# Kernel tuning notes

Measured on AMD Instinct MI355X. Metric: run time of the kernel, lower is better.

Reference implementation:

```python
import jax, jax.numpy as jnp
import numpy as np

N = 50000      # nodes
E = 800000     # edges (avg degree 16)
F_IN = 64      # node_feature_space
H = 64         # hidden_dim
G = 16         # graphs in batch
BN_EPS = 1e-5


def setup_inputs() -> dict:
    key = jax.random.key(0)
    ks = jax.random.split(key, 8)
    x = jax.random.normal(ks[0], (N, F_IN), jnp.float32)
    edge_index = jax.random.randint(ks[1], (2, E), 0, N, dtype=jnp.int64)
    batch = jnp.sort(jax.random.randint(ks[2], (N,), 0, G, dtype=jnp.int64))
    init = lambda k, shp, fan: jax.random.normal(k, shp, jnp.float32) / np.float32(np.sqrt(fan))
    params = dict(
        W1_0=init(ks[3], (F_IN, H), F_IN), b1_0=jnp.zeros((H,), jnp.float32),
        W2_0=init(ks[4], (H, H), H),       b2_0=jnp.zeros((H,), jnp.float32),
        g_0=jnp.ones((H,), jnp.float32),   be_0=jnp.zeros((H,), jnp.float32),
        W1_1=init(ks[5], (H, H), H),       b1_1=jnp.zeros((H,), jnp.float32),
        W2_1=init(ks[6], (H, H), H),       b2_1=jnp.zeros((H,), jnp.float32),
        g_1=jnp.ones((H,), jnp.float32),   be_1=jnp.zeros((H,), jnp.float32),
    )
    return dict(x=x, edge_index=edge_index, batch=batch, **params)


def _gin_layer(x, src, dst, W1, b1, W2, b2, g, be):
    # GINConv (eps=0): h_i = MLP(x_i + sum_{j->i} x_j)
    agg = jax.ops.segment_sum(x[src], dst, num_segments=N)   # [N, d]
    h = x + agg
    h = jnp.maximum(h @ W1 + b1, 0.0) @ W2 + b2              # Linear-ReLU-Linear
    # BatchNorm1d (training-mode batch stats, biased variance as in torch)
    mu = h.mean(axis=0)
    var = h.var(axis=0)
    h = (h - mu) * jax.lax.rsqrt(var + BN_EPS) * g + be
    return jnp.maximum(h, 0.0)                               # ReLU


def reference(x, edge_index, batch,
              W1_0, b1_0, W2_0, b2_0, g_0, be_0,
              W1_1, b1_1, W2_1, b2_1, g_1, be_1):
    src, dst = edge_index[0], edge_index[1]
    x = _gin_layer(x, src, dst, W1_0, b1_0, W2_0, b2_0, g_0, be_0)
    x = _gin_layer(x, src, dst, W1_1, b1_1, W2_1, b2_1, g_1, be_1)
    # global_mean_pool over graph ids
    cnt = jax.ops.segment_sum(jnp.ones((N,), x.dtype), batch, num_segments=G)
    sums = jax.ops.segment_sum(x, batch, num_segments=G)
    h_graph = sums / jnp.maximum(cnt, 1.0)[:, None]
    return (x, h_graph)
```

## Files before the change

kernel.cpp:

```cpp
#include <hip/hip_runtime.h>
#include <hip/hip_bf16.h>


constexpr int NN = 50000;
constexpr int NE = 800000;
constexpr int HD = 64;
constexpr int NG = 16;
constexpr float BN_EPS = 1e-5f;
constexpr int SCAN_BLOCKS = (NN + 255) / 256;
constexpr int NBUCK = (NN + 1023) / 1024;
constexpr int BIN1_BLOCKS = (NE + 4095) / 4096;

__global__ __launch_bounds__(256)
void count_kernel(const int* __restrict__ ei, int* __restrict__ cnt) {
    int e = blockIdx.x * 256 + threadIdx.x;
    if (e >= NE) return;
    atomicAdd(&cnt[ei[NE + e]], 1);
}

__global__ __launch_bounds__(256)
void scan1_kernel(const int* __restrict__ cnt, int* __restrict__ row_ptr,
                  int* __restrict__ partials) {
    int i = blockIdx.x * 256 + threadIdx.x;
    int v = (i < NN) ? cnt[i] : 0;
    __shared__ int s[256];
    s[threadIdx.x] = v;
    __syncthreads();
#pragma unroll
    for (int off = 1; off < 256; off <<= 1) {
        int add = (threadIdx.x >= off) ? s[threadIdx.x - off] : 0;
        __syncthreads();
        s[threadIdx.x] += add;
        __syncthreads();
    }
    if (i < NN) row_ptr[i] = s[threadIdx.x] - v;
    if (threadIdx.x == 255) partials[blockIdx.x] = s[255];
}

__global__ __launch_bounds__(256)
void scan3_kernel(int* __restrict__ row_ptr, const int* __restrict__ partials,
                  int* __restrict__ gcur) {
    __shared__ int s[256];
    __shared__ int orig[256];
    int v = (threadIdx.x < SCAN_BLOCKS) ? partials[threadIdx.x] : 0;
    s[threadIdx.x] = v;
    orig[threadIdx.x] = v;
    __syncthreads();
#pragma unroll
    for (int off = 1; off < 256; off <<= 1) {
        int add = (threadIdx.x >= off) ? s[threadIdx.x - off] : 0;
        __syncthreads();
        s[threadIdx.x] += add;
        __syncthreads();
    }
    int poff = s[blockIdx.x] - orig[blockIdx.x];
    int i = blockIdx.x * 256 + threadIdx.x;
    if (i < NN) {
        int rv = row_ptr[i] + poff;
        row_ptr[i] = rv;
        if ((i & 1023) == 0) gcur[i >> 10] = rv;
    }
    if (i == 0) row_ptr[NN] = NE;
}

__global__ __launch_bounds__(256)
void bin1_kernel(const int* __restrict__ ei, int* __restrict__ gcur,
                 int2* __restrict__ part) {
    __shared__ int lcnt[NBUCK];
    __shared__ int lbase[NBUCK];
    __shared__ int lcur[NBUCK];
    int tid = threadIdx.x;
    int chunk = blockIdx.x * 4096;
    if (tid < NBUCK) lcnt[tid] = 0;
    __syncthreads();
#pragma unroll
    for (int r = 0; r < 16; r++) {
        int e = chunk + r * 256 + tid;
        if (e < NE) atomicAdd(&lcnt[ei[NE + e] >> 10], 1);
    }
    __syncthreads();
    if (tid < NBUCK) {
        lbase[tid] = atomicAdd(&gcur[tid], lcnt[tid]);
        lcur[tid] = 0;
    }
    __syncthreads();
#pragma unroll
    for (int r = 0; r < 16; r++) {
        int e = chunk + r * 256 + tid;
        if (e < NE) {
            int src = ei[e];
            int b = ei[NE + e] >> 10;
            int slot = atomicAdd(&lcur[b], 1);
            part[lbase[b] + slot] = make_int2(src, ei[NE + e]);
        }
    }
}

__global__ __launch_bounds__(256)
void bin2_kernel(const int2* __restrict__ part, const int* __restrict__ row_ptr,
                 int* __restrict__ csr) {
    __shared__ int lcur[1024];
    int b = blockIdx.x;
    int base_row = b << 10;
    for (int i = threadIdx.x; i < 1024; i += 256)
        lcur[i] = row_ptr[min(base_row + i, NN)];
    __syncthreads();
    int s = row_ptr[min(base_row, NN)];
    int e = row_ptr[min(base_row + 1024, NN)];
    for (int i = s + threadIdx.x; i < e; i += 256) {
        int2 p = part[i];
        int pos = atomicAdd(&lcur[p.y & 1023], 1);
        csr[pos] = p.x;
    }
}

__global__ __launch_bounds__(256)
void x2bf_kernel(const float* __restrict__ x, __hip_bfloat16* __restrict__ xb,
                 int* __restrict__ cnt) {
    int i4 = blockIdx.x * 256 + threadIdx.x;
    if (i4 < NN) cnt[i4] = 0;
    if (i4 >= NN * HD / 4) return;
    float4 v = *(const float4*)(x + (size_t)i4 * 4);
    union { ushort4 u; __hip_bfloat16 b[4]; } p;
    p.b[0] = __float2bfloat16(v.x);
    p.b[1] = __float2bfloat16(v.y);
    p.b[2] = __float2bfloat16(v.z);
    p.b[3] = __float2bfloat16(v.w);
    *(ushort4*)((unsigned short*)xb + (size_t)i4 * 4) = p.u;
}

__global__ __launch_bounds__(256)
void agg_kernel(const float* __restrict__ x, const __hip_bfloat16* __restrict__ xb,
                const int* __restrict__ row_ptr, const int* __restrict__ csr,
                float* __restrict__ h, float* __restrict__ stats) {
    if (blockIdx.x == 0 && threadIdx.x < 128) stats[threadIdx.x] = 0.f;
    int row = blockIdx.x * 4 + (threadIdx.x >> 6);
    int lane = threadIdx.x & 63;
    int s = row_ptr[row], e = row_ptr[row + 1];
    int cnt = e - s;
    int ids = (lane < cnt) ? csr[s + lane] : 0;
    float acc = x[(size_t)row * HD + lane];
    int m = min(cnt, 64);
    int j = 0;
    float a0 = 0.f, a1 = 0.f, a2 = 0.f, a3 = 0.f;
    float a4 = 0.f, a5 = 0.f, a6 = 0.f, a7 = 0.f;
    for (; j + 8 <= m; j += 8) {
        int nb0 = __shfl(ids, j);
        int nb1 = __shfl(ids, j + 1);
        int nb2 = __shfl(ids, j + 2);
        int nb3 = __shfl(ids, j + 3);
        int nb4 = __shfl(ids, j + 4);
        int nb5 = __shfl(ids, j + 5);
        int nb6 = __shfl(ids, j + 6);
        int nb7 = __shfl(ids, j + 7);
        float v0 = __bfloat162float(xb[(size_t)nb0 * HD + lane]);
        float v1 = __bfloat162float(xb[(size_t)nb1 * HD + lane]);
        float v2 = __bfloat162float(xb[(size_t)nb2 * HD + lane]);
        float v3 = __bfloat162float(xb[(size_t)nb3 * HD + lane]);
        float v4 = __bfloat162float(xb[(size_t)nb4 * HD + lane]);
        float v5 = __bfloat162float(xb[(size_t)nb5 * HD + lane]);
        float v6 = __bfloat162float(xb[(size_t)nb6 * HD + lane]);
        float v7 = __bfloat162float(xb[(size_t)nb7 * HD + lane]);
        a0 += v0; a1 += v1; a2 += v2; a3 += v3;
        a4 += v4; a5 += v5; a6 += v6; a7 += v7;
    }
    acc += ((a0 + a1) + (a2 + a3)) + ((a4 + a5) + (a6 + a7));
    for (; j < m; j++) {
        int nb = __shfl(ids, j);
        acc += __bfloat162float(xb[(size_t)nb * HD + lane]);
    }
    for (int jj = s + 64; jj < e; jj++) {
        acc += __bfloat162float(xb[(size_t)csr[jj] * HD + lane]);
    }
    h[(size_t)row * HD + lane] = acc;
}

__global__ __launch_bounds__(256)
void mlp_kernel(const float* __restrict__ hin, float* __restrict__ hout,
                const float* __restrict__ W1, const float* __restrict__ b1,
                const float* __restrict__ W2, const float* __restrict__ b2,
                float* __restrict__ stats, float* __restrict__ psums) {
    __shared__ float sh[128 * 65];
    __shared__ float sW[64 * 64];
    __shared__ float sb[64];
    __shared__ float red[2][4][64];
    int tid = threadIdx.x;
    int base = blockIdx.x * 128;

    if (blockIdx.x == 0) {
        float4 z = make_float4(0.f, 0.f, 0.f, 0.f);
        *(float4*)(psums + tid * 4) = z;
    }
    for (int i = tid; i < 4096; i += 256) sW[i] = W1[i];
    if (tid < 64) sb[tid] = b1[tid];
#pragma unroll
    for (int i = 0; i < 8; i++) {
        int i4 = tid + 256 * i;
        int row = i4 >> 4, col = (i4 & 15) * 4;
        int grow = base + row;
        float4 v = (grow < NN) ? *(const float4*)(hin + (size_t)grow * HD + col)
                               : make_float4(0.f, 0.f, 0.f, 0.f);
        float* d = sh + row * 65 + col;
        d[0] = v.x; d[1] = v.y; d[2] = v.z; d[3] = v.w;
    }
    __syncthreads();

    int wv = tid >> 6;
    int lane = tid & 63;

    float acc0[16], acc1[16];
#pragma unroll
    for (int j = 0; j < 16; j++) { acc0[j] = sb[wv * 16 + j]; acc1[j] = acc0[j]; }
    for (int k = 0; k < 64; k++) {
        float a0 = sh[lane * 65 + k];
        float a1 = sh[(64 + lane) * 65 + k];
        const float4* wr = (const float4*)(sW + k * 64 + wv * 16);
#pragma unroll
        for (int q = 0; q < 4; q++) {
            float4 w = wr[q];
            acc0[4 * q + 0] = fmaf(a0, w.x, acc0[4 * q + 0]);
            acc0[4 * q + 1] = fmaf(a0, w.y, acc0[4 * q + 1]);
            acc0[4 * q + 2] = fmaf(a0, w.z, acc0[4 * q + 2]);
            acc0[4 * q + 3] = fmaf(a0, w.w, acc0[4 * q + 3]);
            acc1[4 * q + 0] = fmaf(a1, w.x, acc1[4 * q + 0]);
            acc1[4 * q + 1] = fmaf(a1, w.y, acc1[4 * q + 1]);
            acc1[4 * q + 2] = fmaf(a1, w.z, acc1[4 * q + 2]);
            acc1[4 * q + 3] = fmaf(a1, w.w, acc1[4 * q + 3]);
        }
    }
    __syncthreads();

#pragma unroll
    for (int j = 0; j < 16; j++) {
        sh[lane * 65 + wv * 16 + j] = fmaxf(acc0[j], 0.f);
        sh[(64 + lane) * 65 + wv * 16 + j] = fmaxf(acc1[j], 0.f);
    }
    for (int i = tid; i < 4096; i += 256) sW[i] = W2[i];
    if (tid < 64) sb[tid] = b2[tid];
    __syncthreads();

#pragma unroll
    for (int j = 0; j < 16; j++) { acc0[j] = sb[wv * 16 + j]; acc1[j] = acc0[j]; }
    for (int k = 0; k < 64; k++) {
        float a0 = sh[lane * 65 + k];
        float a1 = sh[(64 + lane) * 65 + k];
        const float4* wr = (const float4*)(sW + k * 64 + wv * 16);
#pragma unroll
        for (int q = 0; q < 4; q++) {
            float4 w = wr[q];
            acc0[4 * q + 0] = fmaf(a0, w.x, acc0[4 * q + 0]);
            acc0[4 * q + 1] = fmaf(a0, w.y, acc0[4 * q + 1]);
            acc0[4 * q + 2] = fmaf(a0, w.z, acc0[4 * q + 2]);
            acc0[4 * q + 3] = fmaf(a0, w.w, acc0[4 * q + 3]);
            acc1[4 * q + 0] = fmaf(a1, w.x, acc1[4 * q + 0]);
            acc1[4 * q + 1] = fmaf(a1, w.y, acc1[4 * q + 1]);
            acc1[4 * q + 2] = fmaf(a1, w.z, acc1[4 * q + 2]);
            acc1[4 * q + 3] = fmaf(a1, w.w, acc1[4 * q + 3]);
        }
    }
    __syncthreads();
#pragma unroll
    for (int j = 0; j < 16; j++) {
        sh[lane * 65 + wv * 16 + j] = acc0[j];
        sh[(64 + lane) * 65 + wv * 16 + j] = acc1[j];
    }
    __syncthreads();

#pragma unroll
    for (int i = 0; i < 8; i++) {
        int i4 = tid + 256 * i;
        int row = i4 >> 4, col = (i4 & 15) * 4;
        int grow = base + row;
        if (grow < NN) {
            const float* s = sh + row * 65 + col;
            *(float4*)(hout + (size_t)grow * HD + col) =
                make_float4(s[0], s[1], s[2], s[3]);
        }
    }

    {
        int col = tid & 63;
        int r0 = (tid >> 6) * 32;
        float s = 0.f, ss = 0.f;
#pragma unroll
        for (int r = 0; r < 32; r++) {
            float v = (base + r0 + r < NN) ? sh[(r0 + r) * 65 + col] : 0.f;
            s += v;
            ss += v * v;
        }
        red[0][tid >> 6][col] = s;
        red[1][tid >> 6][col] = ss;
        __syncthreads();
        if (tid < 64) {
            float S = red[0][0][col] + red[0][1][col] + red[0][2][col] + red[0][3][col];
            atomicAdd(stats + col, S);
        } else if (tid < 128) {
            float SS = red[1][0][col] + red[1][1][col] + red[1][2][col] + red[1][3][col];
            atomicAdd(stats + 64 + col, SS);
        }
    }
}

__global__ __launch_bounds__(256)
void norm_kernel(float* h, const float* __restrict__ stats,
                 const float* __restrict__ g, const float* __restrict__ be,
                 __hip_bfloat16* __restrict__ xb) {
    size_t i4 = (size_t)blockIdx.x * 256 + threadIdx.x;
    if (i4 >= (size_t)NN * HD / 4) return;
    size_t off = i4 * 4;
    int col = (int)(off & 63);
    float4 v = *(const float4*)(h + off);
    float4 sm = *(const float4*)(stats + col);
    float4 sq = *(const float4*)(stats + 64 + col);
    float4 gg = *(const float4*)(g + col);
    float4 bb = *(const float4*)(be + col);
    const float inv = 1.f / (float)NN;
    float4 o;
    {
        float mu = sm.x * inv, var = sq.x * inv - mu * mu;
        float sc = gg.x * rsqrtf(var + BN_EPS);
        o.x = fmaxf((v.x - mu) * sc + bb.x, 0.f);
    }
    {
        float mu = sm.y * inv, var = sq.y * inv - mu * mu;
        float sc = gg.y * rsqrtf(var + BN_EPS);
        o.y = fmaxf((v.y - mu) * sc + bb.y, 0.f);
    }
    {
        float mu = sm.z * inv, var = sq.z * inv - mu * mu;
        float sc = gg.z * rsqrtf(var + BN_EPS);
        o.z = fmaxf((v.z - mu) * sc + bb.z, 0.f);
    }
    {
        float mu = sm.w * inv, var = sq.w * inv - mu * mu;
        float sc = gg.w * rsqrtf(var + BN_EPS);
        o.w = fmaxf((v.w - mu) * sc + bb.w, 0.f);
    }
    *(float4*)(h + off) = o;
    union { ushort4 u; __hip_bfloat16 b[4]; } p;
    p.b[0] = __float2bfloat16(o.x);
    p.b[1] = __float2bfloat16(o.y);
    p.b[2] = __float2bfloat16(o.z);
    p.b[3] = __float2bfloat16(o.w);
    *(ushort4*)((unsigned short*)xb + off) = p.u;
}

__global__ __launch_bounds__(256)
void pool_partial_kernel(const float* __restrict__ x, const int* __restrict__ batch,
                         float* __restrict__ sums) {
    int col = threadIdx.x & 63;
    int rl = threadIdx.x >> 6;
    int rs = blockIdx.x * 250;
    int re = rs + 250;
    int cur = -1;
    float acc = 0.f;
    for (int r = rs + rl; r < re; r += 4) {
        int g = batch[r];
        float v = x[(size_t)r * HD + col];
        if (g != cur) {
            if (cur >= 0) atomicAdd(&sums[cur * HD + col], acc);
            cur = g;
            acc = v;
        } else {
            acc += v;
        }
    }
    if (cur >= 0) atomicAdd(&sums[cur * HD + col], acc);
}

__device__ __forceinline__ int lower_bound_batch(const int* __restrict__ b, int val) {
    int lo = 0, hi = NN;
    while (lo < hi) {
        int mid = (lo + hi) >> 1;
        if (b[mid] < val) lo = mid + 1;
        else hi = mid;
    }
    return lo;
}

__global__ __launch_bounds__(1024)
void pool_finalize_kernel(const float* __restrict__ sums, const int* __restrict__ batch,
                          float* __restrict__ out) {
    int g = threadIdx.x >> 6;
    int col = threadIdx.x & 63;
    int s = lower_bound_batch(batch, g);
    int e = lower_bound_batch(batch, g + 1);
    float cnt = (float)(e - s);
    out[g * HD + col] = sums[g * HD + col] / fmaxf(cnt, 1.f);
}

extern "C" void kernel_launch(void* const* d_in, const int* in_sizes, int n_in,
                              void* d_out, int out_size, void* d_ws, size_t ws_size,
                              hipStream_t stream) {
    const float* x = (const float*)d_in[0];
    const int* ei = (const int*)d_in[1];
    const int* batch = (const int*)d_in[2];
    const float* W1_0 = (const float*)d_in[3];
    const float* b1_0 = (const float*)d_in[4];
    const float* W2_0 = (const float*)d_in[5];
    const float* b2_0 = (const float*)d_in[6];
    const float* g_0 = (const float*)d_in[7];
    const float* be_0 = (const float*)d_in[8];
    const float* W1_1 = (const float*)d_in[9];
    const float* b1_1 = (const float*)d_in[10];
    const float* W2_1 = (const float*)d_in[11];
    const float* b2_1 = (const float*)d_in[12];
    const float* g_1 = (const float*)d_in[13];
    const float* be_1 = (const float*)d_in[14];

    float* out = (float*)d_out;

    float* buf_h = (float*)d_ws;
    float* stats = buf_h + (size_t)NN * HD;
    float* psums = stats + 128;
    int* row_ptr = (int*)(psums + 1024);
    int* cnt = row_ptr + (NN + 2);
    int* partials = cnt + NN;
    int* gcur = partials + 256;
    int* csr = gcur + 64;
    __hip_bfloat16* xb = (__hip_bfloat16*)(csr + NE);
    int2* part = (int2*)(xb + (size_t)NN * HD);

    dim3 b256(256);
    int mlp_grid = (NN + 127) / 128;
    int norm_grid = (NN * HD / 4 + 255) / 256;
    int egrid = (NE + 255) / 256;
    int agg_grid = NN / 4;

    x2bf_kernel<<<norm_grid, b256, 0, stream>>>(x, xb, cnt);
    count_kernel<<<egrid, b256, 0, stream>>>(ei, cnt);
    scan1_kernel<<<SCAN_BLOCKS, b256, 0, stream>>>(cnt, row_ptr, partials);
    scan3_kernel<<<SCAN_BLOCKS, b256, 0, stream>>>(row_ptr, partials, gcur);
    bin1_kernel<<<BIN1_BLOCKS, b256, 0, stream>>>(ei, gcur, part);
    bin2_kernel<<<NBUCK, b256, 0, stream>>>(part, row_ptr, csr);

    agg_kernel<<<agg_grid, b256, 0, stream>>>(x, xb, row_ptr, csr, buf_h, stats);
    mlp_kernel<<<mlp_grid, b256, 0, stream>>>(buf_h, out, W1_0, b1_0, W2_0, b2_0, stats, psums);
    norm_kernel<<<norm_grid, b256, 0, stream>>>(out, stats, g_0, be_0, xb);

    agg_kernel<<<agg_grid, b256, 0, stream>>>(out, xb, row_ptr, csr, buf_h, stats);
    mlp_kernel<<<mlp_grid, b256, 0, stream>>>(buf_h, out, W1_1, b1_1, W2_1, b2_1, stats, psums);
    norm_kernel<<<norm_grid, b256, 0, stream>>>(out, stats, g_1, be_1, xb);

    pool_partial_kernel<<<200, b256, 0, stream>>>(out, batch, psums);
    pool_finalize_kernel<<<1, dim3(1024), 0, stream>>>(psums, batch, out + (size_t)NN * HD);
}
```

Before: 329.3 us.

## Fuse layer-0 batchnorm into second aggregation and merge scan and pool kernels

The first layer's BatchNorm+ReLU is no longer a separate pass. The MLP now writes raw bf16 activations, and the second aggregation kernel applies the per-column scale, offset and ReLU to each gathered neighbor and to the self row. The two-pass scan becomes a single 1024-thread block scan, the edge count kernel reads four edges per thread, and the pool finalize step folds into the pool kernel through a last-block counter. This removes one full read-write pass over the node features and several launches, at the cost of redundant normalization math per gathered edge and a serial single-block scan.

```diff
diff --git a/kernel.cpp b/kernel.cpp
--- a/kernel.cpp
+++ b/kernel.cpp
@@ -7,112 +7,8 @@
 constexpr int HD = 64;
 constexpr int NG = 16;
 constexpr float BN_EPS = 1e-5f;
-constexpr int SCAN_BLOCKS = (NN + 255) / 256;
 constexpr int NBUCK = (NN + 1023) / 1024;
 constexpr int BIN1_BLOCKS = (NE + 4095) / 4096;
-
-__global__ __launch_bounds__(256)
-void count_kernel(const int* __restrict__ ei, int* __restrict__ cnt) {
-    int e = blockIdx.x * 256 + threadIdx.x;
-    if (e >= NE) return;
-    atomicAdd(&cnt[ei[NE + e]], 1);
-}
-
-__global__ __launch_bounds__(256)
-void scan1_kernel(const int* __restrict__ cnt, int* __restrict__ row_ptr,
-                  int* __restrict__ partials) {
-    int i = blockIdx.x * 256 + threadIdx.x;
-    int v = (i < NN) ? cnt[i] : 0;
-    __shared__ int s[256];
-    s[threadIdx.x] = v;
-    __syncthreads();
-#pragma unroll
-    for (int off = 1; off < 256; off <<= 1) {
-        int add = (threadIdx.x >= off) ? s[threadIdx.x - off] : 0;
-        __syncthreads();
-        s[threadIdx.x] += add;
-        __syncthreads();
-    }
-    if (i < NN) row_ptr[i] = s[threadIdx.x] - v;
-    if (threadIdx.x == 255) partials[blockIdx.x] = s[255];
-}
-
-__global__ __launch_bounds__(256)
-void scan3_kernel(int* __restrict__ row_ptr, const int* __restrict__ partials,
-                  int* __restrict__ gcur) {
-    __shared__ int s[256];
-    __shared__ int orig[256];
-    int v = (threadIdx.x < SCAN_BLOCKS) ? partials[threadIdx.x] : 0;
-    s[threadIdx.x] = v;
-    orig[threadIdx.x] = v;
-    __syncthreads();
-#pragma unroll
-    for (int off = 1; off < 256; off <<= 1) {
-        int add = (threadIdx.x >= off) ? s[threadIdx.x - off] : 0;
-        __syncthreads();
-        s[threadIdx.x] += add;
-        __syncthreads();
-    }
-    int poff = s[blockIdx.x] - orig[blockIdx.x];
-    int i = blockIdx.x * 256 + threadIdx.x;
-    if (i < NN) {
-        int rv = row_ptr[i] + poff;
-        row_ptr[i] = rv;
-        if ((i & 1023) == 0) gcur[i >> 10] = rv;
-    }
-    if (i == 0) row_ptr[NN] = NE;
-}
-
-__global__ __launch_bounds__(256)
-void bin1_kernel(const int* __restrict__ ei, int* __restrict__ gcur,
-                 int2* __restrict__ part) {
-    __shared__ int lcnt[NBUCK];
-    __shared__ int lbase[NBUCK];
-    __shared__ int lcur[NBUCK];
-    int tid = threadIdx.x;
-    int chunk = blockIdx.x * 4096;
-    if (tid < NBUCK) lcnt[tid] = 0;
-    __syncthreads();
-#pragma unroll
-    for (int r = 0; r < 16; r++) {
-        int e = chunk + r * 256 + tid;
-        if (e < NE) atomicAdd(&lcnt[ei[NE + e] >> 10], 1);
-    }
-    __syncthreads();
-    if (tid < NBUCK) {
-        lbase[tid] = atomicAdd(&gcur[tid], lcnt[tid]);
-        lcur[tid] = 0;
-    }
-    __syncthreads();
-#pragma unroll
-    for (int r = 0; r < 16; r++) {
-        int e = chunk + r * 256 + tid;
-        if (e < NE) {
-            int src = ei[e];
-            int b = ei[NE + e] >> 10;
-            int slot = atomicAdd(&lcur[b], 1);
-            part[lbase[b] + slot] = make_int2(src, ei[NE + e]);
-        }
-    }
-}
-
-__global__ __launch_bounds__(256)
-void bin2_kernel(const int2* __restrict__ part, const int* __restrict__ row_ptr,
-                 int* __restrict__ csr) {
-    __shared__ int lcur[1024];
-    int b = blockIdx.x;
-    int base_row = b << 10;
-    for (int i = threadIdx.x; i < 1024; i += 256)
-        lcur[i] = row_ptr[min(base_row + i, NN)];
-    __syncthreads();
-    int s = row_ptr[min(base_row, NN)];
-    int e = row_ptr[min(base_row + 1024, NN)];
-    for (int i = s + threadIdx.x; i < e; i += 256) {
-        int2 p = part[i];
-        int pos = atomicAdd(&lcur[p.y & 1023], 1);
-        csr[pos] = p.x;
-    }
-}
 
 __global__ __launch_bounds__(256)
 void x2bf_kernel(const float* __restrict__ x, __hip_bfloat16* __restrict__ xb,
@@ -127,6 +23,102 @@
     p.b[2] = __float2bfloat16(v.z);
     p.b[3] = __float2bfloat16(v.w);
     *(ushort4*)((unsigned short*)xb + (size_t)i4 * 4) = p.u;
+}
+
+__global__ __launch_bounds__(256)
+void count_kernel(const int* __restrict__ ei, int* __restrict__ cnt) {
+    int e4 = (blockIdx.x * 256 + threadIdx.x) * 4;
+    if (e4 >= NE) return;
+    int4 d = *(const int4*)(ei + NE + e4);
+    atomicAdd(&cnt[d.x], 1);
+    atomicAdd(&cnt[d.y], 1);
+    atomicAdd(&cnt[d.z], 1);
+    atomicAdd(&cnt[d.w], 1);
+}
+
+__global__ __launch_bounds__(1024)
+void scan_kernel(const int* __restrict__ cnt, int* __restrict__ row_ptr,
+                 int* __restrict__ gcur) {
+    __shared__ int sums[1024];
+    int t = threadIdx.x;
+    const int C = 49;
+    int base = t * C;
+    int s = 0;
+    for (int i = 0; i < C; i++) {
+        int idx = base + i;
+        s += (idx < NN) ? cnt[idx] : 0;
+    }
+    sums[t] = s;
+    __syncthreads();
+    for (int off = 1; off < 1024; off <<= 1) {
+        int add = (t >= off) ? sums[t - off] : 0;
+        __syncthreads();
+        sums[t] += add;
+        __syncthreads();
+    }
+    int run = sums[t] - s;
+    for (int i = 0; i < C; i++) {
+        int idx = base + i;
+        if (idx < NN) {
+            int c = cnt[idx];
+            row_ptr[idx] = run;
+            if ((idx & 1023) == 0) gcur[idx >> 10] = run;
+            run += c;
+        }
+    }
+    if (t == 1023) row_ptr[NN] = NE;
+}
+
+__global__ __launch_bounds__(256)
+void bin1_kernel(const int* __restrict__ ei, int* __restrict__ gcur,
+                 int2* __restrict__ part) {
+    __shared__ int lcnt[NBUCK];
+    __shared__ int lbase[NBUCK];
+    __shared__ int lcur[NBUCK];
+    int tid = threadIdx.x;
+    int chunk = blockIdx.x * 4096;
+    if (tid < NBUCK) lcnt[tid] = 0;
+    __syncthreads();
+#pragma unroll
+    for (int r = 0; r < 16; r++) {
+        int e = chunk + r * 256 + tid;
+        if (e < NE) atomicAdd(&lcnt[ei[NE + e] >> 10], 1);
+    }
+    __syncthreads();
+    if (tid < NBUCK) {
+        lbase[tid] = atomicAdd(&gcur[tid], lcnt[tid]);
+        lcur[tid] = 0;
+    }
+    __syncthreads();
+#pragma unroll
+    for (int r = 0; r < 16; r++) {
+        int e = chunk + r * 256 + tid;
+        if (e < NE) {
+            int src = ei[e];
+            int dst = ei[NE + e];
+            int b = dst >> 10;
+            int slot = atomicAdd(&lcur[b], 1);
+            part[lbase[b] + slot] = make_int2(src, dst);
+        }
+    }
+}
+
+__global__ __launch_bounds__(256)
+void bin2_kernel(const int2* __restrict__ part, const int* __restrict__ row_ptr,
+                 int* __restrict__ csr) {
+    __shared__ int lcur[1024];
+    int b = blockIdx.x;
+    int base_row = b << 10;
+    for (int i = threadIdx.x; i < 1024; i += 256)
+        lcur[i] = row_ptr[min(base_row + i, NN)];
+    __syncthreads();
+    int s = row_ptr[min(base_row, NN)];
+    int e = row_ptr[min(base_row + 1024, NN)];
+    for (int i = s + threadIdx.x; i < e; i += 256) {
+        int2 p = part[i];
+        int pos = atomicAdd(&lcur[p.y & 1023], 1);
+        csr[pos] = p.x;
+    }
 }
 
 __global__ __launch_bounds__(256)
@@ -153,16 +145,14 @@
         int nb5 = __shfl(ids, j + 5);
         int nb6 = __shfl(ids, j + 6);
         int nb7 = __shfl(ids, j + 7);
-        float v0 = __bfloat162float(xb[(size_t)nb0 * HD + lane]);
-        float v1 = __bfloat162float(xb[(size_t)nb1 * HD + lane]);
-        float v2 = __bfloat162float(xb[(size_t)nb2 * HD + lane]);
-        float v3 = __bfloat162float(xb[(size_t)nb3 * HD + lane]);
-        float v4 = __bfloat162float(xb[(size_t)nb4 * HD + lane]);
-        float v5 = __bfloat162float(xb[(size_t)nb5 * HD + lane]);
-        float v6 = __bfloat162float(xb[(size_t)nb6 * HD + lane]);
-        float v7 = __bfloat162float(xb[(size_t)nb7 * HD + lane]);
-        a0 += v0; a1 += v1; a2 += v2; a3 += v3;
-        a4 += v4; a5 += v5; a6 += v6; a7 += v7;
+        a0 += __bfloat162float(xb[(size_t)nb0 * HD + lane]);
+        a1 += __bfloat162float(xb[(size_t)nb1 * HD + lane]);
+        a2 += __bfloat162float(xb[(size_t)nb2 * HD + lane]);
+        a3 += __bfloat162float(xb[(size_t)nb3 * HD + lane]);
+        a4 += __bfloat162float(xb[(size_t)nb4 * HD + lane]);
+        a5 += __bfloat162float(xb[(size_t)nb5 * HD + lane]);
+        a6 += __bfloat162float(xb[(size_t)nb6 * HD + lane]);
+        a7 += __bfloat162float(xb[(size_t)nb7 * HD + lane]);
     }
     acc += ((a0 + a1) + (a2 + a3)) + ((a4 + a5) + (a6 + a7));
     for (; j < m; j++) {
@@ -176,10 +166,72 @@
 }
 
 __global__ __launch_bounds__(256)
+void aggn_kernel(const float* __restrict__ hraw, const __hip_bfloat16* __restrict__ xbr,
+                 const int* __restrict__ row_ptr, const int* __restrict__ csr,
+                 const float* __restrict__ stats_prev, const float* __restrict__ g0,
+                 const float* __restrict__ be0,
+                 float* __restrict__ h, float* __restrict__ stats_next) {
+    if (blockIdx.x == 0 && threadIdx.x < 128) stats_next[threadIdx.x] = 0.f;
+    int row = blockIdx.x * 4 + (threadIdx.x >> 6);
+    int lane = threadIdx.x & 63;
+    const float inv = 1.f / (float)NN;
+    float mu = stats_prev[lane] * inv;
+    float var = stats_prev[64 + lane] * inv - mu * mu;
+    float sc = g0[lane] * rsqrtf(var + BN_EPS);
+    float off = be0[lane] - mu * sc;
+    int s = row_ptr[row], e = row_ptr[row + 1];
+    int cnt = e - s;
+    int ids = (lane < cnt) ? csr[s + lane] : 0;
+    float acc = fmaxf(fmaf(hraw[(size_t)row * HD + lane], sc, off), 0.f);
+    int m = min(cnt, 64);
+    int j = 0;
+    float a0 = 0.f, a1 = 0.f, a2 = 0.f, a3 = 0.f;
+    float a4 = 0.f, a5 = 0.f, a6 = 0.f, a7 = 0.f;
+    for (; j + 8 <= m; j += 8) {
+        int nb0 = __shfl(ids, j);
+        int nb1 = __shfl(ids, j + 1);
+        int nb2 = __shfl(ids, j + 2);
+        int nb3 = __shfl(ids, j + 3);
+        int nb4 = __shfl(ids, j + 4);
+        int nb5 = __shfl(ids, j + 5);
+        int nb6 = __shfl(ids, j + 6);
+        int nb7 = __shfl(ids, j + 7);
+        float v0 = __bfloat162float(xbr[(size_t)nb0 * HD + lane]);
+        float v1 = __bfloat162float(xbr[(size_t)nb1 * HD + lane]);
+        float v2 = __bfloat162float(xbr[(size_t)nb2 * HD + lane]);
+        float v3 = __bfloat162float(xbr[(size_t)nb3 * HD + lane]);
+        float v4 = __bfloat162float(xbr[(size_t)nb4 * HD + lane]);
+        float v5 = __bfloat162float(xbr[(size_t)nb5 * HD + lane]);
+        float v6 = __bfloat162float(xbr[(size_t)nb6 * HD + lane]);
+        float v7 = __bfloat162float(xbr[(size_t)nb7 * HD + lane]);
+        a0 += fmaxf(fmaf(v0, sc, off), 0.f);
+        a1 += fmaxf(fmaf(v1, sc, off), 0.f);
+        a2 += fmaxf(fmaf(v2, sc, off), 0.f);
+        a3 += fmaxf(fmaf(v3, sc, off), 0.f);
+        a4 += fmaxf(fmaf(v4, sc, off), 0.f);
+        a5 += fmaxf(fmaf(v5, sc, off), 0.f);
+        a6 += fmaxf(fmaf(v6, sc, off), 0.f);
+        a7 += fmaxf(fmaf(v7, sc, off), 0.f);
+    }
+    acc += ((a0 + a1) + (a2 + a3)) + ((a4 + a5) + (a6 + a7));
+    for (; j < m; j++) {
+        int nb = __shfl(ids, j);
+        float v = __bfloat162float(xbr[(size_t)nb * HD + lane]);
+        acc += fmaxf(fmaf(v, sc, off), 0.f);
+    }
+    for (int jj = s + 64; jj < e; jj++) {
+        float v = __bfloat162float(xbr[(size_t)csr[jj] * HD + lane]);
+        acc += fmaxf(fmaf(v, sc, off), 0.f);
+    }
+    h[(size_t)row * HD + lane] = acc;
+}
+
+__global__ __launch_bounds__(256)
 void mlp_kernel(const float* __restrict__ hin, float* __restrict__ hout,
                 const float* __restrict__ W1, const float* __restrict__ b1,
                 const float* __restrict__ W2, const float* __restrict__ b2,
-                float* __restrict__ stats, float* __restrict__ psums) {
+                float* __restrict__ stats, float* __restrict__ psums,
+                int* __restrict__ pctr, __hip_bfloat16* __restrict__ xbr) {
     __shared__ float sh[128 * 65];
     __shared__ float sW[64 * 64];
     __shared__ float sb[64];
@@ -190,6 +242,7 @@
     if (blockIdx.x == 0) {
         float4 z = make_float4(0.f, 0.f, 0.f, 0.f);
         *(float4*)(psums + tid * 4) = z;
+        if (tid == 0) pctr[0] = 0;
     }
     for (int i = tid; i < 4096; i += 256) sW[i] = W1[i];
     if (tid < 64) sb[tid] = b1[tid];
@@ -273,8 +326,16 @@
         int grow = base + row;
         if (grow < NN) {
             const float* s = sh + row * 65 + col;
-            *(float4*)(hout + (size_t)grow * HD + col) =
-                make_float4(s[0], s[1], s[2], s[3]);
+            float4 v = make_float4(s[0], s[1], s[2], s[3]);
+            *(float4*)(hout + (size_t)grow * HD + col) = v;
+            if (xbr) {
+                union { ushort4 u; __hip_bfloat16 b[4]; } p;
+                p.b[0] = __float2bfloat16(v.x);
+                p.b[1] = __float2bfloat16(v.y);
+                p.b[2] = __float2bfloat16(v.z);
+                p.b[3] = __float2bfloat16(v.w);
+                *(ushort4*)((unsigned short*)xbr + (size_t)grow * HD + col) = p.u;
+            }
         }
     }
 
@@ -303,8 +364,7 @@
 
 __global__ __launch_bounds__(256)
 void norm_kernel(float* h, const float* __restrict__ stats,
-                 const float* __restrict__ g, const float* __restrict__ be,
-                 __hip_bfloat16* __restrict__ xb) {
+                 const float* __restrict__ g, const float* __restrict__ be) {
     size_t i4 = (size_t)blockIdx.x * 256 + threadIdx.x;
     if (i4 >= (size_t)NN * HD / 4) return;
     size_t off = i4 * 4;
@@ -337,17 +397,22 @@
         o.w = fmaxf((v.w - mu) * sc + bb.w, 0.f);
     }
     *(float4*)(h + off) = o;
-    union { ushort4 u; __hip_bfloat16 b[4]; } p;
-    p.b[0] = __float2bfloat16(o.x);
-    p.b[1] = __float2bfloat16(o.y);
-    p.b[2] = __float2bfloat16(o.z);
-    p.b[3] = __float2bfloat16(o.w);
-    *(ushort4*)((unsigned short*)xb + off) = p.u;
-}
-
-__global__ __launch_bounds__(256)
-void pool_partial_kernel(const float* __restrict__ x, const int* __restrict__ batch,
-                         float* __restrict__ sums) {
+}
+
+__device__ __forceinline__ int lower_bound_batch(const int* __restrict__ b, int val) {
+    int lo = 0, hi = NN;
+    while (lo < hi) {
+        int mid = (lo + hi) >> 1;
+        if (b[mid] < val) lo = mid + 1;
+        else hi = mid;
+    }
+    return lo;
+}
+
+__global__ __launch_bounds__(256)
+void pool_kernel(const float* __restrict__ x, const int* __restrict__ batch,
+                 float* __restrict__ sums, int* __restrict__ pctr,
+                 float* __restrict__ out) {
     int col = threadIdx.x & 63;
     int rl = threadIdx.x >> 6;
     int rs = blockIdx.x * 250;
@@ -366,27 +431,20 @@
         }
     }
     if (cur >= 0) atomicAdd(&sums[cur * HD + col], acc);
-}
-
-__device__ __forceinline__ int lower_bound_batch(const int* __restrict__ b, int val) {
-    int lo = 0, hi = NN;
-    while (lo < hi) {
-        int mid = (lo + hi) >> 1;
-        if (b[mid] < val) lo = mid + 1;
-        else hi = mid;
-    }
-    return lo;
-}
-
-__global__ __launch_bounds__(1024)
-void pool_finalize_kernel(const float* __restrict__ sums, const int* __restrict__ batch,
-                          float* __restrict__ out) {
-    int g = threadIdx.x >> 6;
-    int col = threadIdx.x & 63;
-    int s = lower_bound_batch(batch, g);
-    int e = lower_bound_batch(batch, g + 1);
-    float cnt = (float)(e - s);
-    out[g * HD + col] = sums[g * HD + col] / fmaxf(cnt, 1.f);
+
+    __threadfence();
+    __shared__ int last;
+    if (threadIdx.x == 0) last = (atomicAdd(pctr, 1) == gridDim.x - 1);
+    __syncthreads();
+    if (!last) return;
+    __threadfence();
+    for (int i = threadIdx.x; i < NG * HD; i += 256) {
+        int g = i >> 6;
+        float sum = atomicAdd(&sums[i], 0.0f);
+        int s = lower_bound_batch(batch, g);
+        int e = lower_bound_batch(batch, g + 1);
+        out[i] = sum / fmaxf((float)(e - s), 1.f);
+    }
 }
 
 extern "C" void kernel_launch(void* const* d_in, const int* in_sizes, int n_in,
@@ -411,12 +469,13 @@
     float* out = (float*)d_out;
 
     float* buf_h = (float*)d_ws;
-    float* stats = buf_h + (size_t)NN * HD;
-    float* psums = stats + 128;
-    int* row_ptr = (int*)(psums + 1024);
+    float* stats0 = buf_h + (size_t)NN * HD;
+    float* stats1 = stats0 + 128;
+    float* psums = stats1 + 128;
+    int* pctr = (int*)(psums + 1024);
+    int* row_ptr = pctr + 64;
     int* cnt = row_ptr + (NN + 2);
-    int* partials = cnt + NN;
-    int* gcur = partials + 256;
+    int* gcur = cnt + NN;
     int* csr = gcur + 64;
     __hip_bfloat16* xb = (__hip_bfloat16*)(csr + NE);
     int2* part = (int2*)(xb + (size_t)NN * HD);
@@ -424,24 +483,24 @@
     dim3 b256(256);
     int mlp_grid = (NN + 127) / 128;
     int norm_grid = (NN * HD / 4 + 255) / 256;
-    int egrid = (NE + 255) / 256;
+    int cnt_grid = (NE / 4 + 255) / 256;
     int agg_grid = NN / 4;
 
     x2bf_kernel<<<norm_grid, b256, 0, stream>>>(x, xb, cnt);
-    count_kernel<<<egrid, b256, 0, stream>>>(ei, cnt);
-    scan1_kernel<<<SCAN_BLOCKS, b256, 0, stream>>>(cnt, row_ptr, partials);
-    scan3_kernel<<<SCAN_BLOCKS, b256, 0, stream>>>(row_ptr, partials, gcur);
+    count_kernel<<<cnt_grid, b256, 0, stream>>>(ei, cnt);
+    scan_kernel<<<1, dim3(1024), 0, stream>>>(cnt, row_ptr, gcur);
     bin1_kernel<<<BIN1_BLOCKS, b256, 0, stream>>>(ei, gcur, part);
     bin2_kernel<<<NBUCK, b256, 0, stream>>>(part, row_ptr, csr);
 
-    agg_kernel<<<agg_grid, b256, 0, stream>>>(x, xb, row_ptr, csr, buf_h, stats);
-    mlp_kernel<<<mlp_grid, b256, 0, stream>>>(buf_h, out, W1_0, b1_0, W2_0, b2_0, stats, psums);
-    norm_kernel<<<norm_grid, b256, 0, stream>>>(out, stats, g_0, be_0, xb);
-
-    agg_kernel<<<agg_grid, b256, 0, stream>>>(out, xb, row_ptr, csr, buf_h, stats);
-    mlp_kernel<<<mlp_grid, b256, 0, stream>>>(buf_h, out, W1_1, b1_1, W2_1, b2_1, stats, psums);
-    norm_kernel<<<norm_grid, b256, 0, stream>>>(out, stats, g_1, be_1, xb);
-
-    pool_partial_kernel<<<200, b256, 0, stream>>>(out, batch, psums);
-    pool_finalize_kernel<<<1, dim3(1024), 0, stream>>>(psums, batch, out + (size_t)NN * HD);
-}
+    agg_kernel<<<agg_grid, b256, 0, stream>>>(x, xb, row_ptr, csr, buf_h, stats0);
+    mlp_kernel<<<mlp_grid, b256, 0, stream>>>(buf_h, out, W1_0, b1_0, W2_0, b2_0,
+                                              stats0, psums, pctr, xb);
+
+    aggn_kernel<<<agg_grid, b256, 0, stream>>>(out, xb, row_ptr, csr,
+                                               stats0, g_0, be_0, buf_h, stats1);
+    mlp_kernel<<<mlp_grid, b256, 0, stream>>>(buf_h, out, W1_1, b1_1, W2_1, b2_1,
+                                              stats1, psums, pctr, (__hip_bfloat16*)nullptr);
+    norm_kernel<<<norm_grid, b256, 0, stream>>>(out, stats1, g_1, be_1);
+
+    pool_kernel<<<200, b256, 0, stream>>>(out, batch, psums, pctr, out + (size_t)NN * HD);
+}
```

After: 437.6 us. +32.9%, slower.
